# Performance work log

Measured on AMD Instinct MI355X. Metric: run time of the kernel, lower is better.

## Reference

```python
import jax, jax.numpy as jnp
import numpy as np

B, S, D, H = 2, 2048, 2048, 16
HD = D // H  # head_dim = 128
ROPE_BASE = 10000.0


def _rope_tables(seq_len, head_dim, base, dtype):
    inv_freq = 1.0 / (base ** (jnp.arange(0, head_dim, 2, dtype=jnp.float32) / head_dim))
    t = jnp.arange(seq_len, dtype=jnp.float32)
    freqs = jnp.einsum('s,d->sd', t, inv_freq)           # [S, HD/2]
    emb = jnp.concatenate([freqs, freqs], axis=-1)        # [S, HD]
    return jnp.cos(emb).astype(dtype), jnp.sin(emb).astype(dtype)


def _rotate_half(x):
    half = x.shape[-1] // 2
    return jnp.concatenate([-x[..., half:], x[..., :half]], axis=-1)


def setup_inputs() -> dict:
    key = jax.random.key(0)
    kx, kq, kk, kv, ko = jax.random.split(key, 5)
    std = 0.02
    return {
        'x': jax.random.normal(kx, (B, S, D), dtype=jnp.float32),
        'Wq': jax.random.normal(kq, (D, D), dtype=jnp.float32) * std,
        'Wk': jax.random.normal(kk, (D, D), dtype=jnp.float32) * std,
        'Wv': jax.random.normal(kv, (D, D), dtype=jnp.float32) * std,
        'Wo': jax.random.normal(ko, (D, D), dtype=jnp.float32) * std,
    }


def reference(x, Wq, Wk, Wv, Wo):
    b, s, d = x.shape
    scale = HD ** -0.5
    # projections (nn.Linear: x @ W.T), split heads -> [b, h, s, hd]
    q = (x @ Wq.T).reshape(b, s, H, HD).transpose(0, 2, 1, 3)
    k = (x @ Wk.T).reshape(b, s, H, HD).transpose(0, 2, 1, 3)
    v = (x @ Wv.T).reshape(b, s, H, HD).transpose(0, 2, 1, 3)
    cos, sin = _rope_tables(s, HD, ROPE_BASE, x.dtype)    # [s, hd]
    q = q * cos + _rotate_half(q) * sin
    k = k * cos + _rotate_half(k) * sin
    scores = jnp.einsum('bhqd,bhkd->bhqk', q, k) * scale  # [b,h,s,s]
    causal = jnp.triu(jnp.ones((s, s), dtype=bool), k=1)
    scores = jnp.where(causal, jnp.float32(-jnp.inf).astype(scores.dtype), scores)
    attn = jax.nn.softmax(scores, axis=-1)
    out = jnp.einsum('bhqk,bhkd->bhqd', attn, v)
    out = out.transpose(0, 2, 1, 3).reshape(b, s, d)
    return out @ Wo.T
```

## Files before the change

### kernel.cpp

```cpp
#include <hip/hip_runtime.h>
#include <hip/hip_bf16.h>
#include <cstdint>
#include <cstddef>

#define B_ 2
#define S_ 2048
#define D_ 2048
#define H_ 16
#define HD_ 128

typedef __bf16 bf16_t;
typedef __bf16 bf16x8 __attribute__((ext_vector_type(8)));
typedef __bf16 bf16x4 __attribute__((ext_vector_type(4)));
typedef short s16x4 __attribute__((ext_vector_type(4)));
typedef float f32x4 __attribute__((ext_vector_type(4)));

__device__ __forceinline__ void async16(const bf16_t* g, bf16_t* l) {
    __builtin_amdgcn_global_load_lds(
        (const __attribute__((address_space(1))) unsigned int*)g,
        (__attribute__((address_space(3))) unsigned int*)l, 16, 0, 0);
}

__device__ __forceinline__ f32x4 mfma16x16x16_bf16(bf16x4 a, bf16x4 b, f32x4 c) {
#if __has_builtin(__builtin_amdgcn_mfma_f32_16x16x16_bf16)
    return __builtin_amdgcn_mfma_f32_16x16x16_bf16(a, b, c, 0, 0, 0);
#elif __has_builtin(__builtin_amdgcn_mfma_f32_16x16x16bf16_1k)
    return __builtin_amdgcn_mfma_f32_16x16x16bf16_1k(
        __builtin_bit_cast(s16x4, a), __builtin_bit_cast(s16x4, b), c, 0, 0, 0);
#else
    f32x4 d = c;
    asm("v_mfma_f32_16x16x16_bf16 %0, %1, %2, %0" : "+v"(d) : "v"(a), "v"(b));
    return d;
#endif
}

__global__ void f2b_multi(const float* __restrict__ x, const float* __restrict__ wq,
                          const float* __restrict__ wk, const float* __restrict__ wv,
                          const float* __restrict__ wo, bf16_t* __restrict__ xb,
                          bf16_t* __restrict__ wqb, bf16_t* __restrict__ wkb,
                          bf16_t* __restrict__ wvb, bf16_t* __restrict__ wob) {
    const float* in; bf16_t* out;
    float sc = 1.0f;
    switch (blockIdx.y) {
        case 0: in = x;            out = xb;            break;
        case 1: in = x + 4194304;  out = xb + 4194304;  break;
        case 2: in = wq;           out = wqb; sc = 0.08838834764831845f; break;
        case 3: in = wk;           out = wkb;           break;
        case 4: in = wv;           out = wvb;           break;
        default: in = wo;          out = wob;           break;
    }
    int i = (blockIdx.x * blockDim.x + threadIdx.x) * 4;
    float4 v = *(const float4*)(in + i);
    bf16x4 o = { (bf16_t)(v.x * sc), (bf16_t)(v.y * sc), (bf16_t)(v.z * sc), (bf16_t)(v.w * sc) };
    *(bf16x4*)(out + i) = o;
}

__global__ void rope_kernel(bf16_t* __restrict__ q, bf16_t* __restrict__ k) {
    int idx = blockIdx.x * blockDim.x + threadIdx.x;
    bf16_t* p = (blockIdx.y == 0) ? q : k;
    int i0 = (idx & 7) * 8;
    int rest = idx >> 3;
    int h = rest & (H_ - 1);
    int row = rest >> 4;
    int s = row & (S_ - 1);
    size_t base = (size_t)row * D_ + (size_t)h * HD_ + i0;
    bf16x8 x0 = *(bf16x8*)(p + base);
    bf16x8 x1 = *(bf16x8*)(p + base + 64);
    bf16x8 o0, o1;
#pragma unroll
    for (int j = 0; j < 8; ++j) {
        float inv = __expf(-(float)(i0 + j) * 0.14391156831212787f);
        float ang = (float)s * inv;
        float sn, c;
        __sincosf(ang, &sn, &c);
        float a = (float)x0[j], bb = (float)x1[j];
        o0[j] = (bf16_t)(a * c - bb * sn);
        o1[j] = (bf16_t)(bb * c + a * sn);
    }
    *(bf16x8*)(p + base) = o0;
    *(bf16x8*)(p + base + 64) = o1;
}


__global__ __launch_bounds__(256) void gemm_qkv(const bf16_t* __restrict__ A,
                                                const bf16_t* __restrict__ Wq,
                                                const bf16_t* __restrict__ Wk,
                                                const bf16_t* __restrict__ Wv,
                                                bf16_t* __restrict__ qb,
                                                bf16_t* __restrict__ kb,
                                                bf16_t* __restrict__ vtb) {
    __shared__ __align__(16) bf16_t As[128 * 64];
    __shared__ __align__(16) bf16_t Bs[128 * 64];
    const int K = D_;
    int t = threadIdx.x;
    int w = t >> 6, lane = t & 63, lo = lane & 15, hi = lane >> 4;
    int seg = blockIdx.x >> 4;
    int n0 = (blockIdx.x & 15) * 128;
    int m0 = blockIdx.y * 128;
    const bf16_t* Bt = (seg == 0) ? Wq : (seg == 1) ? Wk : Wv;
    int wm = (w & 1) * 64, wn = (w >> 1) * 64;
    f32x4 acc[4][4] = {};
    int srow = w * 32 + (lane >> 3);
    int scol = ((lane & 7) ^ (lane >> 3)) * 8;
    const bf16_t* gA = A  + (size_t)(m0 + srow) * K + scol;
    const bf16_t* gB = Bt + (size_t)(n0 + srow) * K + scol;
    bf16_t* lA = As + w * 2048 + lane * 8;
    bf16_t* lB = Bs + w * 2048 + lane * 8;
    for (int k0 = 0; k0 < K; k0 += 64) {
#pragma unroll
        for (int i = 0; i < 4; ++i) {
            async16(gA + (size_t)(i * 8) * K + k0, lA + i * 512);
            async16(gB + (size_t)(i * 8) * K + k0, lB + i * 512);
        }
        __syncthreads();
#pragma unroll
        for (int kk = 0; kk < 2; ++kk) {
            bf16x8 af[4], bfr[4];
            int pc = (kk * 4 + hi) ^ (lo & 7);
#pragma unroll
            for (int ms = 0; ms < 4; ++ms)
                af[ms] = *(const bf16x8*)(As + (wm + ms * 16 + lo) * 64 + pc * 8);
#pragma unroll
            for (int ns = 0; ns < 4; ++ns)
                bfr[ns] = *(const bf16x8*)(Bs + (wn + ns * 16 + lo) * 64 + pc * 8);
#pragma unroll
            for (int ms = 0; ms < 4; ++ms)
#pragma unroll
                for (int ns = 0; ns < 4; ++ns)
                    acc[ms][ns] = __builtin_amdgcn_mfma_f32_16x16x32_bf16(af[ms], bfr[ns], acc[ms][ns], 0, 0, 0);
        }
        __syncthreads();
    }
    if (seg < 2) {
        bf16_t* C = (seg == 0) ? qb : kb;
#pragma unroll
        for (int ms = 0; ms < 4; ++ms)
#pragma unroll
            for (int ns = 0; ns < 4; ++ns)
#pragma unroll
                for (int r = 0; r < 4; ++r)
                    C[(size_t)(m0 + wm + ms * 16 + hi * 4 + r) * D_ + n0 + wn + ns * 16 + lo] = (bf16_t)acc[ms][ns][r];
    } else {
#pragma unroll
        for (int ms = 0; ms < 4; ++ms) {
            int mrow = m0 + wm + ms * 16 + hi * 4;
            int bb = mrow >> 11, s = mrow & (S_ - 1);
#pragma unroll
            for (int ns = 0; ns < 4; ++ns) {
                int d = n0 + wn + ns * 16 + lo;
                bf16x4 pv = { (bf16_t)acc[ms][ns][0], (bf16_t)acc[ms][ns][1],
                              (bf16_t)acc[ms][ns][2], (bf16_t)acc[ms][ns][3] };
                *(bf16x4*)(vtb + (size_t)bb * D_ * S_ + (size_t)d * S_ + s) = pv;
            }
        }
    }
}

__global__ __launch_bounds__(256) void gemm_bt_f32(const bf16_t* __restrict__ A,
                                                   const bf16_t* __restrict__ Bt,
                                                   float* __restrict__ C,
                                                   int M, int N, int K) {
    __shared__ __align__(16) bf16_t As[128 * 64];
    __shared__ __align__(16) bf16_t Bs[128 * 64];
    int t = threadIdx.x;
    int w = t >> 6, lane = t & 63, lo = lane & 15, hi = lane >> 4;
    int m0 = blockIdx.y * 128, n0 = blockIdx.x * 128;
    int wm = (w & 1) * 64, wn = (w >> 1) * 64;
    f32x4 acc[4][4] = {};
    int srow = w * 32 + (lane >> 3);
    int scol = ((lane & 7) ^ (lane >> 3)) * 8;
    const bf16_t* gA = A  + (size_t)(m0 + srow) * K + scol;
    const bf16_t* gB = Bt + (size_t)(n0 + srow) * K + scol;
    bf16_t* lA = As + w * 2048 + lane * 8;
    bf16_t* lB = Bs + w * 2048 + lane * 8;
    for (int k0 = 0; k0 < K; k0 += 64) {
#pragma unroll
        for (int i = 0; i < 4; ++i) {
            async16(gA + (size_t)(i * 8) * K + k0, lA + i * 512);
            async16(gB + (size_t)(i * 8) * K + k0, lB + i * 512);
        }
        __syncthreads();
#pragma unroll
        for (int kk = 0; kk < 2; ++kk) {
            bf16x8 af[4], bfr[4];
            int pc = (kk * 4 + hi) ^ (lo & 7);
#pragma unroll
            for (int ms = 0; ms < 4; ++ms)
                af[ms] = *(const bf16x8*)(As + (wm + ms * 16 + lo) * 64 + pc * 8);
#pragma unroll
            for (int ns = 0; ns < 4; ++ns)
                bfr[ns] = *(const bf16x8*)(Bs + (wn + ns * 16 + lo) * 64 + pc * 8);
#pragma unroll
            for (int ms = 0; ms < 4; ++ms)
#pragma unroll
                for (int ns = 0; ns < 4; ++ns)
                    acc[ms][ns] = __builtin_amdgcn_mfma_f32_16x16x32_bf16(af[ms], bfr[ns], acc[ms][ns], 0, 0, 0);
        }
        __syncthreads();
    }
#pragma unroll
    for (int ms = 0; ms < 4; ++ms)
#pragma unroll
        for (int ns = 0; ns < 4; ++ns)
#pragma unroll
            for (int r = 0; r < 4; ++r)
                C[(size_t)(m0 + wm + ms * 16 + hi * 4 + r) * N + n0 + wn + ns * 16 + lo] = acc[ms][ns][r];
}

__global__ __launch_bounds__(256) void attn_kernel(const bf16_t* __restrict__ q,
                                                   const bf16_t* __restrict__ k,
                                                   const bf16_t* __restrict__ vt,
                                                   bf16_t* __restrict__ o) {
    __shared__ __align__(16) bf16_t Ks[128 * 128];
    __shared__ __align__(16) bf16_t Vs[128 * 128];
    int t = threadIdx.x;
    int w = t >> 6, lane = t & 63, lo = lane & 15, hi = lane >> 4;
    int bx = blockIdx.x;
    int b = blockIdx.y >> 4, h = blockIdx.y & 15;
    const size_t head_off = (size_t)b * S_ * D_ + (size_t)h * HD_;
    const size_t vhead_off = ((size_t)b * D_ + (size_t)h * HD_) * S_;

#pragma unroll 1
    for (int pass = 0; pass < 2; ++pass) {
        int qt = pass ? (31 - bx) : bx;
        int q0 = qt * 64;
        int qg = q0 + w * 16 + lo;
        bf16x8 aq[4];
#pragma unroll
        for (int c = 0; c < 4; ++c)
            aq[c] = *(const bf16x8*)(q + head_off + (size_t)qg * D_ + c * 32 + hi * 8);

        float l_part = 0.f;
        f32x4 oacc[8] = {};
        int nkt = (qt >> 1) + 1;
        for (int kt = 0; kt < nkt; ++kt) {
            int k0 = kt * 128;
            __syncthreads();
#pragma unroll
            for (int i = 0; i < 8; ++i) {
                int chunk = w * 8 + i;
                int r = chunk * 4 + (lane >> 4);
                int lc = (lane & 15) ^ (r & 15);
                async16(k + head_off + (size_t)(k0 + r) * D_ + lc * 8,
                        Ks + chunk * 512 + lane * 8);
            }
#pragma unroll
            for (int i = 0; i < 8; ++i) {
                int chunk = w * 8 + i;
                int d = chunk * 4 + (lane >> 4);
                int lc = (lane & 15) ^ (d & 15);
                async16(vt + vhead_off + (size_t)d * S_ + k0 + lc * 8,
                        Vs + chunk * 512 + lane * 8);
            }
            __syncthreads();

            if (k0 <= q0 + w * 16 + 15) {
                f32x4 sacc[8] = {};
#pragma unroll
                for (int c = 0; c < 4; ++c) {
#pragma unroll
                    for (int nt = 0; nt < 8; ++nt) {
                        int row = nt * 16 + lo;
                        int pc = (c * 4 + hi) ^ lo;
                        bf16x8 ak = *(const bf16x8*)(Ks + row * 128 + pc * 8);
                        sacc[nt] = __builtin_amdgcn_mfma_f32_16x16x32_bf16(ak, aq[c], sacc[nt], 0, 0, 0);
                    }
                }
                bool diag = (k0 + 127 > q0 + w * 16);
                bf16x4 pf[8];
#pragma unroll
                for (int nt = 0; nt < 8; ++nt) {
#pragma unroll
                    for (int r = 0; r < 4; ++r) {
                        float e = __expf(fminf(sacc[nt][r], 60.f));
                        if (diag) {
                            int kg = k0 + nt * 16 + hi * 4 + r;
                            if (kg > qg) e = 0.f;
                        }
                        l_part += e;
                        pf[nt][r] = (bf16_t)e;
                    }
                }
#pragma unroll
                for (int nt = 0; nt < 8; ++nt) {
                    int kkb = nt * 16 + hi * 4;
                    int c16 = kkb >> 3, rem = kkb & 7;
#pragma unroll
                    for (int dt = 0; dt < 8; ++dt) {
                        int d = dt * 16 + lo;
                        bf16x4 av = *(const bf16x4*)(Vs + d * 128 + (c16 ^ (d & 15)) * 8 + rem);
                        oacc[dt] = mfma16x16x16_bf16(av, pf[nt], oacc[dt]);
                    }
                }
            }
        }
        float l = l_part;
        l += __shfl_xor(l, 16);
        l += __shfl_xor(l, 32);
        float rl = 1.0f / l;
#pragma unroll
        for (int dt = 0; dt < 8; ++dt) {
            bf16x4 ov = { (bf16_t)(oacc[dt][0] * rl), (bf16_t)(oacc[dt][1] * rl),
                          (bf16_t)(oacc[dt][2] * rl), (bf16_t)(oacc[dt][3] * rl) };
            *(bf16x4*)(o + head_off + (size_t)qg * D_ + dt * 16 + hi * 4) = ov;
        }
    }
}

extern "C" void kernel_launch(void* const* d_in, const int* in_sizes, int n_in,
                              void* d_out, int out_size, void* d_ws, size_t ws_size,
                              hipStream_t stream) {
    (void)in_sizes; (void)n_in; (void)out_size; (void)ws_size;
    const float* x  = (const float*)d_in[0];
    const float* Wq = (const float*)d_in[1];
    const float* Wk = (const float*)d_in[2];
    const float* Wv = (const float*)d_in[3];
    const float* Wo = (const float*)d_in[4];
    char* ws = (char*)d_ws;
    bf16_t* xb  = (bf16_t*)(ws);
    bf16_t* Wqb = (bf16_t*)(ws + 16777216);
    bf16_t* Wkb = (bf16_t*)(ws + 25165824);
    bf16_t* Wvb = (bf16_t*)(ws + 33554432);
    bf16_t* Wob = (bf16_t*)(ws + 41943040);
    bf16_t* qb  = (bf16_t*)(ws + 50331648);
    bf16_t* kb  = (bf16_t*)(ws + 67108864);
    bf16_t* vtb = (bf16_t*)(ws + 83886080);
    bf16_t* ob  = (bf16_t*)(ws + 100663296);
    float* out = (float*)d_out;

    f2b_multi<<<dim3(4096, 6), 256, 0, stream>>>(x, Wq, Wk, Wv, Wo, xb, Wqb, Wkb, Wvb, Wob);

    gemm_qkv<<<dim3(48, 32), 256, 0, stream>>>(xb, Wqb, Wkb, Wvb, qb, kb, vtb);

    rope_kernel<<<dim3((B_ * S_ * H_ * 8) / 256, 2), 256, 0, stream>>>(qb, kb);

    attn_kernel<<<dim3(16, B_ * H_), 256, 0, stream>>>(qb, kb, vtb, ob);

    gemm_bt_f32<<<dim3(D_ / 128, (B_ * S_) / 128), 256, 0, stream>>>(ob, Wob, out, B_ * S_, D_, D_);
}
```

Baseline: 384.3 us.

## Double-buffer projection GEMMs with 256x128 tiles and 8-wave blocks

Rewrites both projection GEMM kernels to use 512-thread blocks computing 256x128 output tiles, with a two-stage LDS double buffer fed by async global-to-LDS loads. Explicit vmcnt/lgkmcnt waits, barriers and setprio around the MFMA bursts let the next K-tile's loads overlap with current compute. The aim is to hide global load latency and improve operand reuse per block. In exchange it uses 96KB of LDS per block, fewer blocks in the grid, and relies on hand-placed waits whose counts must match the number of loads issued per stage.

```diff
diff --git a/kernel.cpp b/kernel.cpp
--- a/kernel.cpp
+++ b/kernel.cpp
@@ -82,72 +82,117 @@
 }
 
 
-__global__ __launch_bounds__(256) void gemm_qkv(const bf16_t* __restrict__ A,
-                                                const bf16_t* __restrict__ Wq,
-                                                const bf16_t* __restrict__ Wk,
-                                                const bf16_t* __restrict__ Wv,
-                                                bf16_t* __restrict__ qb,
-                                                bf16_t* __restrict__ kb,
-                                                bf16_t* __restrict__ vtb) {
-    __shared__ __align__(16) bf16_t As[128 * 64];
-    __shared__ __align__(16) bf16_t Bs[128 * 64];
+__global__ __launch_bounds__(512, 2) void gemm_qkv(const bf16_t* __restrict__ A,
+                                                   const bf16_t* __restrict__ Wq,
+                                                   const bf16_t* __restrict__ Wk,
+                                                   const bf16_t* __restrict__ Wv,
+                                                   bf16_t* __restrict__ qb,
+                                                   bf16_t* __restrict__ kb,
+                                                   bf16_t* __restrict__ vtb) {
+    __shared__ __align__(16) bf16_t lds[49152];
     const int K = D_;
+    const int NT = K / 64;
     int t = threadIdx.x;
     int w = t >> 6, lane = t & 63, lo = lane & 15, hi = lane >> 4;
     int seg = blockIdx.x >> 4;
     int n0 = (blockIdx.x & 15) * 128;
-    int m0 = blockIdx.y * 128;
+    int m0 = blockIdx.y * 256;
     const bf16_t* Bt = (seg == 0) ? Wq : (seg == 1) ? Wk : Wv;
-    int wm = (w & 1) * 64, wn = (w >> 1) * 64;
-    f32x4 acc[4][4] = {};
-    int srow = w * 32 + (lane >> 3);
+    int wm = w >> 2, wn = w & 3;
+    f32x4 acc[8][2] = {};
+    int srowA = w * 32 + (lane >> 3);
+    int srowB = w * 16 + (lane >> 3);
     int scol = ((lane & 7) ^ (lane >> 3)) * 8;
-    const bf16_t* gA = A  + (size_t)(m0 + srow) * K + scol;
-    const bf16_t* gB = Bt + (size_t)(n0 + srow) * K + scol;
-    bf16_t* lA = As + w * 2048 + lane * 8;
-    bf16_t* lB = Bs + w * 2048 + lane * 8;
-    for (int k0 = 0; k0 < K; k0 += 64) {
-#pragma unroll
-        for (int i = 0; i < 4; ++i) {
-            async16(gA + (size_t)(i * 8) * K + k0, lA + i * 512);
-            async16(gB + (size_t)(i * 8) * K + k0, lB + i * 512);
-        }
-        __syncthreads();
-#pragma unroll
-        for (int kk = 0; kk < 2; ++kk) {
-            bf16x8 af[4], bfr[4];
-            int pc = (kk * 4 + hi) ^ (lo & 7);
+    const bf16_t* gA = A  + (size_t)(m0 + srowA) * K + scol;
+    const bf16_t* gB = Bt + (size_t)(n0 + srowB) * K + scol;
+
+    auto STAGE = [&](int c, int kt) {
+        bf16_t* dA = lds + c * 24576 + w * 2048 + lane * 8;
+        bf16_t* dB = lds + c * 24576 + 16384 + w * 1024 + lane * 8;
+        int k0 = kt * 64;
+#pragma unroll
+        for (int i = 0; i < 4; ++i)
+            async16(gA + (size_t)(i * 8) * K + k0, dA + i * 512);
+#pragma unroll
+        for (int i = 0; i < 2; ++i)
+            async16(gB + (size_t)(i * 8) * K + k0, dB + i * 512);
+    };
+
+    STAGE(0, 0);
+    STAGE(1, 1);
+    asm volatile("s_waitcnt vmcnt(6)" ::: "memory");
+    __builtin_amdgcn_sched_barrier(0);
+    __builtin_amdgcn_s_barrier();
+
+#pragma unroll 1
+    for (int tt = 0; tt < NT; ++tt) {
+        int cur = tt & 1;
+        const bf16_t* As = lds + cur * 24576;
+        const bf16_t* Bs = As + 16384;
+#pragma unroll
+        for (int p = 0; p < 2; ++p) {
+            bf16x8 af[4][2], bfv[2][2];
+#pragma unroll
+            for (int ms = 0; ms < 4; ++ms) {
+                int row = wm * 128 + p * 64 + ms * 16 + lo;
+#pragma unroll
+                for (int kk = 0; kk < 2; ++kk)
+                    af[ms][kk] = *(const bf16x8*)(As + row * 64 + (((kk * 4 + hi) ^ (lo & 7)) * 8));
+            }
+#pragma unroll
+            for (int ns = 0; ns < 2; ++ns) {
+                int row = wn * 32 + ns * 16 + lo;
+#pragma unroll
+                for (int kk = 0; kk < 2; ++kk)
+                    bfv[ns][kk] = *(const bf16x8*)(Bs + row * 64 + (((kk * 4 + hi) ^ (lo & 7)) * 8));
+            }
+            __builtin_amdgcn_sched_barrier(0);
+            __builtin_amdgcn_s_barrier();
+            asm volatile("s_waitcnt lgkmcnt(0)" ::: "memory");
+            __builtin_amdgcn_sched_barrier(0);
+            __builtin_amdgcn_s_setprio(1);
 #pragma unroll
             for (int ms = 0; ms < 4; ++ms)
-                af[ms] = *(const bf16x8*)(As + (wm + ms * 16 + lo) * 64 + pc * 8);
-#pragma unroll
-            for (int ns = 0; ns < 4; ++ns)
-                bfr[ns] = *(const bf16x8*)(Bs + (wn + ns * 16 + lo) * 64 + pc * 8);
-#pragma unroll
-            for (int ms = 0; ms < 4; ++ms)
-#pragma unroll
-                for (int ns = 0; ns < 4; ++ns)
-                    acc[ms][ns] = __builtin_amdgcn_mfma_f32_16x16x32_bf16(af[ms], bfr[ns], acc[ms][ns], 0, 0, 0);
-        }
-        __syncthreads();
-    }
+#pragma unroll
+                for (int ns = 0; ns < 2; ++ns)
+#pragma unroll
+                    for (int kk = 0; kk < 2; ++kk)
+                        acc[p * 4 + ms][ns] = __builtin_amdgcn_mfma_f32_16x16x32_bf16(
+                            af[ms][kk], bfv[ns][kk], acc[p * 4 + ms][ns], 0, 0, 0);
+            __builtin_amdgcn_s_setprio(0);
+            __builtin_amdgcn_sched_barrier(0);
+            __builtin_amdgcn_s_barrier();
+        }
+        if (tt + 2 < NT) {
+            STAGE(cur, tt + 2);
+            asm volatile("s_waitcnt vmcnt(6)" ::: "memory");
+            __builtin_amdgcn_sched_barrier(0);
+            __builtin_amdgcn_s_barrier();
+        } else if (tt + 1 < NT) {
+            asm volatile("s_waitcnt vmcnt(0)" ::: "memory");
+            __builtin_amdgcn_sched_barrier(0);
+            __builtin_amdgcn_s_barrier();
+        }
+    }
+
     if (seg < 2) {
         bf16_t* C = (seg == 0) ? qb : kb;
 #pragma unroll
-        for (int ms = 0; ms < 4; ++ms)
-#pragma unroll
-            for (int ns = 0; ns < 4; ++ns)
+        for (int ms = 0; ms < 8; ++ms)
+#pragma unroll
+            for (int ns = 0; ns < 2; ++ns)
 #pragma unroll
                 for (int r = 0; r < 4; ++r)
-                    C[(size_t)(m0 + wm + ms * 16 + hi * 4 + r) * D_ + n0 + wn + ns * 16 + lo] = (bf16_t)acc[ms][ns][r];
+                    C[(size_t)(m0 + wm * 128 + ms * 16 + hi * 4 + r) * D_ + n0 + wn * 32 + ns * 16 + lo] =
+                        (bf16_t)acc[ms][ns][r];
     } else {
 #pragma unroll
-        for (int ms = 0; ms < 4; ++ms) {
-            int mrow = m0 + wm + ms * 16 + hi * 4;
+        for (int ms = 0; ms < 8; ++ms) {
+            int mrow = m0 + wm * 128 + ms * 16 + hi * 4;
             int bb = mrow >> 11, s = mrow & (S_ - 1);
 #pragma unroll
-            for (int ns = 0; ns < 4; ++ns) {
-                int d = n0 + wn + ns * 16 + lo;
+            for (int ns = 0; ns < 2; ++ns) {
+                int d = n0 + wn * 32 + ns * 16 + lo;
                 bf16x4 pv = { (bf16_t)acc[ms][ns][0], (bf16_t)acc[ms][ns][1],
                               (bf16_t)acc[ms][ns][2], (bf16_t)acc[ms][ns][3] };
                 *(bf16x4*)(vtb + (size_t)bb * D_ * S_ + (size_t)d * S_ + s) = pv;
@@ -156,55 +201,102 @@
     }
 }
 
-__global__ __launch_bounds__(256) void gemm_bt_f32(const bf16_t* __restrict__ A,
-                                                   const bf16_t* __restrict__ Bt,
-                                                   float* __restrict__ C,
-                                                   int M, int N, int K) {
-    __shared__ __align__(16) bf16_t As[128 * 64];
-    __shared__ __align__(16) bf16_t Bs[128 * 64];
+__global__ __launch_bounds__(512, 2) void gemm_bt_f32(const bf16_t* __restrict__ A,
+                                                      const bf16_t* __restrict__ Bt,
+                                                      float* __restrict__ C,
+                                                      int M, int N, int K) {
+    (void)M;
+    __shared__ __align__(16) bf16_t lds[49152];
+    const int NT = K / 64;
     int t = threadIdx.x;
     int w = t >> 6, lane = t & 63, lo = lane & 15, hi = lane >> 4;
-    int m0 = blockIdx.y * 128, n0 = blockIdx.x * 128;
-    int wm = (w & 1) * 64, wn = (w >> 1) * 64;
-    f32x4 acc[4][4] = {};
-    int srow = w * 32 + (lane >> 3);
+    int n0 = blockIdx.x * 128;
+    int m0 = blockIdx.y * 256;
+    int wm = w >> 2, wn = w & 3;
+    f32x4 acc[8][2] = {};
+    int srowA = w * 32 + (lane >> 3);
+    int srowB = w * 16 + (lane >> 3);
     int scol = ((lane & 7) ^ (lane >> 3)) * 8;
-    const bf16_t* gA = A  + (size_t)(m0 + srow) * K + scol;
-    const bf16_t* gB = Bt + (size_t)(n0 + srow) * K + scol;
-    bf16_t* lA = As + w * 2048 + lane * 8;
-    bf16_t* lB = Bs + w * 2048 + lane * 8;
-    for (int k0 = 0; k0 < K; k0 += 64) {
-#pragma unroll
-        for (int i = 0; i < 4; ++i) {
-            async16(gA + (size_t)(i * 8) * K + k0, lA + i * 512);
-            async16(gB + (size_t)(i * 8) * K + k0, lB + i * 512);
-        }
-        __syncthreads();
-#pragma unroll
-        for (int kk = 0; kk < 2; ++kk) {
-            bf16x8 af[4], bfr[4];
-            int pc = (kk * 4 + hi) ^ (lo & 7);
+    const bf16_t* gA = A  + (size_t)(m0 + srowA) * K + scol;
+    const bf16_t* gB = Bt + (size_t)(n0 + srowB) * K + scol;
+
+    auto STAGE = [&](int c, int kt) {
+        bf16_t* dA = lds + c * 24576 + w * 2048 + lane * 8;
+        bf16_t* dB = lds + c * 24576 + 16384 + w * 1024 + lane * 8;
+        int k0 = kt * 64;
+#pragma unroll
+        for (int i = 0; i < 4; ++i)
+            async16(gA + (size_t)(i * 8) * K + k0, dA + i * 512);
+#pragma unroll
+        for (int i = 0; i < 2; ++i)
+            async16(gB + (size_t)(i * 8) * K + k0, dB + i * 512);
+    };
+
+    STAGE(0, 0);
+    STAGE(1, 1);
+    asm volatile("s_waitcnt vmcnt(6)" ::: "memory");
+    __builtin_amdgcn_sched_barrier(0);
+    __builtin_amdgcn_s_barrier();
+
+#pragma unroll 1
+    for (int tt = 0; tt < NT; ++tt) {
+        int cur = tt & 1;
+        const bf16_t* As = lds + cur * 24576;
+        const bf16_t* Bs = As + 16384;
+#pragma unroll
+        for (int p = 0; p < 2; ++p) {
+            bf16x8 af[4][2], bfv[2][2];
+#pragma unroll
+            for (int ms = 0; ms < 4; ++ms) {
+                int row = wm * 128 + p * 64 + ms * 16 + lo;
+#pragma unroll
+                for (int kk = 0; kk < 2; ++kk)
+                    af[ms][kk] = *(const bf16x8*)(As + row * 64 + (((kk * 4 + hi) ^ (lo & 7)) * 8));
+            }
+#pragma unroll
+            for (int ns = 0; ns < 2; ++ns) {
+                int row = wn * 32 + ns * 16 + lo;
+#pragma unroll
+                for (int kk = 0; kk < 2; ++kk)
+                    bfv[ns][kk] = *(const bf16x8*)(Bs + row * 64 + (((kk * 4 + hi) ^ (lo & 7)) * 8));
+            }
+            __builtin_amdgcn_sched_barrier(0);
+            __builtin_amdgcn_s_barrier();
+            asm volatile("s_waitcnt lgkmcnt(0)" ::: "memory");
+            __builtin_amdgcn_sched_barrier(0);
+            __builtin_amdgcn_s_setprio(1);
 #pragma unroll
             for (int ms = 0; ms < 4; ++ms)
-                af[ms] = *(const bf16x8*)(As + (wm + ms * 16 + lo) * 64 + pc * 8);
-#pragma unroll
-            for (int ns = 0; ns < 4; ++ns)
-                bfr[ns] = *(const bf16x8*)(Bs + (wn + ns * 16 + lo) * 64 + pc * 8);
-#pragma unroll
-            for (int ms = 0; ms < 4; ++ms)
-#pragma unroll
-                for (int ns = 0; ns < 4; ++ns)
-                    acc[ms][ns] = __builtin_amdgcn_mfma_f32_16x16x32_bf16(af[ms], bfr[ns], acc[ms][ns], 0, 0, 0);
-        }
-        __syncthreads();
-    }
-#pragma unroll
-    for (int ms = 0; ms < 4; ++ms)
-#pragma unroll
-        for (int ns = 0; ns < 4; ++ns)
+#pragma unroll
+                for (int ns = 0; ns < 2; ++ns)
+#pragma unroll
+                    for (int kk = 0; kk < 2; ++kk)
+                        acc[p * 4 + ms][ns] = __builtin_amdgcn_mfma_f32_16x16x32_bf16(
+                            af[ms][kk], bfv[ns][kk], acc[p * 4 + ms][ns], 0, 0, 0);
+            __builtin_amdgcn_s_setprio(0);
+            __builtin_amdgcn_sched_barrier(0);
+            __builtin_amdgcn_s_barrier();
+        }
+        if (tt + 2 < NT) {
+            STAGE(cur, tt + 2);
+            asm volatile("s_waitcnt vmcnt(6)" ::: "memory");
+            __builtin_amdgcn_sched_barrier(0);
+            __builtin_amdgcn_s_barrier();
+        } else if (tt + 1 < NT) {
+            asm volatile("s_waitcnt vmcnt(0)" ::: "memory");
+            __builtin_amdgcn_sched_barrier(0);
+            __builtin_amdgcn_s_barrier();
+        }
+    }
+
+#pragma unroll
+    for (int ms = 0; ms < 8; ++ms)
+#pragma unroll
+        for (int ns = 0; ns < 2; ++ns)
 #pragma unroll
             for (int r = 0; r < 4; ++r)
-                C[(size_t)(m0 + wm + ms * 16 + hi * 4 + r) * N + n0 + wn + ns * 16 + lo] = acc[ms][ns][r];
+                C[(size_t)(m0 + wm * 128 + ms * 16 + hi * 4 + r) * N + n0 + wn * 32 + ns * 16 + lo] =
+                    acc[ms][ns][r];
 }
 
 __global__ __launch_bounds__(256) void attn_kernel(const bf16_t* __restrict__ q,
@@ -330,11 +422,11 @@
 
     f2b_multi<<<dim3(4096, 6), 256, 0, stream>>>(x, Wq, Wk, Wv, Wo, xb, Wqb, Wkb, Wvb, Wob);
 
-    gemm_qkv<<<dim3(48, 32), 256, 0, stream>>>(xb, Wqb, Wkb, Wvb, qb, kb, vtb);
+    gemm_qkv<<<dim3(48, 16), 512, 0, stream>>>(xb, Wqb, Wkb, Wvb, qb, kb, vtb);
 
     rope_kernel<<<dim3((B_ * S_ * H_ * 8) / 256, 2), 256, 0, stream>>>(qb, kb);
 
     attn_kernel<<<dim3(16, B_ * H_), 256, 0, stream>>>(qb, kb, vtb, ob);
 
-    gemm_bt_f32<<<dim3(D_ / 128, (B_ * S_) / 128), 256, 0, stream>>>(ob, Wob, out, B_ * S_, D_, D_);
-}
+    gemm_bt_f32<<<dim3(D_ / 128, (B_ * S_) / 256), 512, 0, stream>>>(ob, Wob, out, B_ * S_, D_, D_);
+}
```

New measurement: 408.1 us. +6.2%, slower.

## Double-buffer K/V tiles in attention and enlarge query tile to 128 rows

Applied to the files above, without the earlier changes.

The attention kernel now runs 512 threads (8 waves) per block, covering 128 query rows instead of 64, and loads K/V tiles into two LDS buffers so the next tile's async load overlaps compute on the current one. This halves the grid and drops one barrier per iteration, aiming to hide global-load latency and raise K/V reuse per load. LDS use doubles to 128 KB per block, which may limit blocks per CU. Total blocks fall to 256, which could leave some CUs idle.

```diff
diff --git a/kernel.cpp b/kernel.cpp
--- a/kernel.cpp
+++ b/kernel.cpp
@@ -207,12 +207,12 @@
                 C[(size_t)(m0 + wm + ms * 16 + hi * 4 + r) * N + n0 + wn + ns * 16 + lo] = acc[ms][ns][r];
 }
 
-__global__ __launch_bounds__(256) void attn_kernel(const bf16_t* __restrict__ q,
+__global__ __launch_bounds__(512) void attn_kernel(const bf16_t* __restrict__ q,
                                                    const bf16_t* __restrict__ k,
                                                    const bf16_t* __restrict__ vt,
                                                    bf16_t* __restrict__ o) {
-    __shared__ __align__(16) bf16_t Ks[128 * 128];
-    __shared__ __align__(16) bf16_t Vs[128 * 128];
+    __shared__ __align__(16) bf16_t Ks[2][128 * 128];
+    __shared__ __align__(16) bf16_t Vs[2][128 * 128];
     int t = threadIdx.x;
     int w = t >> 6, lane = t & 63, lo = lane & 15, hi = lane >> 4;
     int bx = blockIdx.x;
@@ -222,8 +222,8 @@
 
 #pragma unroll 1
     for (int pass = 0; pass < 2; ++pass) {
-        int qt = pass ? (31 - bx) : bx;
-        int q0 = qt * 64;
+        int qt = pass ? (15 - bx) : bx;
+        int q0 = qt * 128;
         int qg = q0 + w * 16 + lo;
         bf16x8 aq[4];
 #pragma unroll
@@ -232,67 +232,87 @@
 
         float l_part = 0.f;
         f32x4 oacc[8] = {};
-        int nkt = (qt >> 1) + 1;
+        int nkt = qt + 1;
+
+        {
+#pragma unroll
+            for (int i = 0; i < 4; ++i) {
+                int chunk = w * 4 + i;
+                int r = chunk * 4 + hi;
+                async16(k + head_off + (size_t)r * D_ + (lo ^ (r & 15)) * 8,
+                        Ks[0] + chunk * 512 + lane * 8);
+            }
+#pragma unroll
+            for (int i = 0; i < 4; ++i) {
+                int chunk = w * 4 + i;
+                int d = chunk * 4 + hi;
+                async16(vt + vhead_off + (size_t)d * S_ + (lo ^ (d & 15)) * 8,
+                        Vs[0] + chunk * 512 + lane * 8);
+            }
+        }
+        __syncthreads();
+
         for (int kt = 0; kt < nkt; ++kt) {
             int k0 = kt * 128;
+            int cb = kt & 1;
+            if (kt + 1 < nkt) {
+                int kn = k0 + 128;
+#pragma unroll
+                for (int i = 0; i < 4; ++i) {
+                    int chunk = w * 4 + i;
+                    int r = chunk * 4 + hi;
+                    async16(k + head_off + (size_t)(kn + r) * D_ + (lo ^ (r & 15)) * 8,
+                            Ks[cb ^ 1] + chunk * 512 + lane * 8);
+                }
+#pragma unroll
+                for (int i = 0; i < 4; ++i) {
+                    int chunk = w * 4 + i;
+                    int d = chunk * 4 + hi;
+                    async16(vt + vhead_off + (size_t)d * S_ + kn + (lo ^ (d & 15)) * 8,
+                            Vs[cb ^ 1] + chunk * 512 + lane * 8);
+                }
+            }
+
+            const bf16_t* Kb = Ks[cb];
+            const bf16_t* Vb = Vs[cb];
+            f32x4 sacc[8] = {};
+#pragma unroll
+            for (int c = 0; c < 4; ++c) {
+#pragma unroll
+                for (int nt = 0; nt < 8; ++nt) {
+                    int row = nt * 16 + lo;
+                    int pc = (c * 4 + hi) ^ lo;
+                    bf16x8 ak = *(const bf16x8*)(Kb + row * 128 + pc * 8);
+                    sacc[nt] = __builtin_amdgcn_mfma_f32_16x16x32_bf16(ak, aq[c], sacc[nt], 0, 0, 0);
+                }
+            }
+            bool diag = (kt == qt);
+            bf16x4 pf[8];
+#pragma unroll
+            for (int nt = 0; nt < 8; ++nt) {
+#pragma unroll
+                for (int r = 0; r < 4; ++r) {
+                    float e = __expf(fminf(sacc[nt][r], 60.f));
+                    if (diag) {
+                        int kg = k0 + nt * 16 + hi * 4 + r;
+                        if (kg > qg) e = 0.f;
+                    }
+                    l_part += e;
+                    pf[nt][r] = (bf16_t)e;
+                }
+            }
+#pragma unroll
+            for (int nt = 0; nt < 8; ++nt) {
+                int kkb = nt * 16 + hi * 4;
+                int c16 = kkb >> 3, rem = kkb & 7;
+#pragma unroll
+                for (int dt = 0; dt < 8; ++dt) {
+                    int d = dt * 16 + lo;
+                    bf16x4 av = *(const bf16x4*)(Vb + d * 128 + (c16 ^ (d & 15)) * 8 + rem);
+                    oacc[dt] = mfma16x16x16_bf16(av, pf[nt], oacc[dt]);
+                }
+            }
             __syncthreads();
-#pragma unroll
-            for (int i = 0; i < 8; ++i) {
-                int chunk = w * 8 + i;
-                int r = chunk * 4 + (lane >> 4);
-                int lc = (lane & 15) ^ (r & 15);
-                async16(k + head_off + (size_t)(k0 + r) * D_ + lc * 8,
-                        Ks + chunk * 512 + lane * 8);
-            }
-#pragma unroll
-            for (int i = 0; i < 8; ++i) {
-                int chunk = w * 8 + i;
-                int d = chunk * 4 + (lane >> 4);
-                int lc = (lane & 15) ^ (d & 15);
-                async16(vt + vhead_off + (size_t)d * S_ + k0 + lc * 8,
-                        Vs + chunk * 512 + lane * 8);
-            }
-            __syncthreads();
-
-            if (k0 <= q0 + w * 16 + 15) {
-                f32x4 sacc[8] = {};
-#pragma unroll
-                for (int c = 0; c < 4; ++c) {
-#pragma unroll
-                    for (int nt = 0; nt < 8; ++nt) {
-                        int row = nt * 16 + lo;
-                        int pc = (c * 4 + hi) ^ lo;
-                        bf16x8 ak = *(const bf16x8*)(Ks + row * 128 + pc * 8);
-                        sacc[nt] = __builtin_amdgcn_mfma_f32_16x16x32_bf16(ak, aq[c], sacc[nt], 0, 0, 0);
-                    }
-                }
-                bool diag = (k0 + 127 > q0 + w * 16);
-                bf16x4 pf[8];
-#pragma unroll
-                for (int nt = 0; nt < 8; ++nt) {
-#pragma unroll
-                    for (int r = 0; r < 4; ++r) {
-                        float e = __expf(fminf(sacc[nt][r], 60.f));
-                        if (diag) {
-                            int kg = k0 + nt * 16 + hi * 4 + r;
-                            if (kg > qg) e = 0.f;
-                        }
-                        l_part += e;
-                        pf[nt][r] = (bf16_t)e;
-                    }
-                }
-#pragma unroll
-                for (int nt = 0; nt < 8; ++nt) {
-                    int kkb = nt * 16 + hi * 4;
-                    int c16 = kkb >> 3, rem = kkb & 7;
-#pragma unroll
-                    for (int dt = 0; dt < 8; ++dt) {
-                        int d = dt * 16 + lo;
-                        bf16x4 av = *(const bf16x4*)(Vs + d * 128 + (c16 ^ (d & 15)) * 8 + rem);
-                        oacc[dt] = mfma16x16x16_bf16(av, pf[nt], oacc[dt]);
-                    }
-                }
-            }
         }
         float l = l_part;
         l += __shfl_xor(l, 16);
@@ -334,7 +354,7 @@
 
     rope_kernel<<<dim3((B_ * S_ * H_ * 8) / 256, 2), 256, 0, stream>>>(qb, kb);
 
-    attn_kernel<<<dim3(16, B_ * H_), 256, 0, stream>>>(qb, kb, vtb, ob);
+    attn_kernel<<<dim3(8, B_ * H_), 512, 0, stream>>>(qb, kb, vtb, ob);
 
     gemm_bt_f32<<<dim3(D_ / 128, (B_ * S_) / 128), 256, 0, stream>>>(ob, Wob, out, B_ * S_, D_, D_);
 }
```

Result: faster. 371.4 us (-3.3%).
